# Kernel optimization log

Measured on AMD Instinct MI355X. Metric: run time of the kernel, lower is better.

The kernel has to match this reference:

```python
import jax, jax.numpy as jnp
import numpy as np

N = 50000      # nodes
E = 800000     # edges (avg degree 16)
F = 6          # input node features
C = 64         # conv_hidden_channels
M = 256        # mlp_hidden_channels
NCLS = 24      # num_classes
EPS = 1e-5     # BatchNorm eps


def _bn(h, g, b):
    # BatchNorm1d in training mode: biased batch stats over the batch axis
    mu = h.mean(axis=0)
    var = ((h - mu) ** 2).mean(axis=0)
    return g * (h - mu) * jax.lax.rsqrt(var + EPS) + b


def _block(x, W, b, g, beta):
    # Lin -> ReLU -> BN  (one MLP block)
    return _bn(jax.nn.relu(x @ W + b), g, beta)


def _edge_conv(x, src, dst, Wa, ba, ga, bea, Wb, bb, gb, beb):
    # EdgeConv: message = MLP([x_i, x_j - x_i]), max-aggregated onto target i
    xi = x[dst]                                   # [E, d]
    xj = x[src]                                   # [E, d]
    e = jnp.concatenate([xi, xj - xi], axis=-1)   # [E, 2d]
    h = _block(_block(e, Wa, ba, ga, bea), Wb, bb, gb, beb)  # [E, C]
    agg = jax.ops.segment_max(h, dst, num_segments=N)        # [N, C]
    return jnp.where(jnp.isfinite(agg), agg, 0.0)  # zero-fill isolated nodes


def setup_inputs() -> dict:
    key = jax.random.key(0)
    ks = jax.random.split(key, 12)

    def w(k, shape, fan_in):
        return jax.random.normal(k, shape, jnp.float32) * (1.0 / np.sqrt(fan_in))

    z = lambda *s: jnp.zeros(s, jnp.float32)
    o = lambda *s: jnp.ones(s, jnp.float32)

    x = jax.random.normal(ks[0], (N, F), jnp.float32)
    edge_index = jax.random.randint(ks[1], (2, E), 0, N, jnp.int32)

    return {
        "x": x,
        # conv1 MLP: Lin(2F,C)+BN, Lin(C,C)+BN
        "W1a": w(ks[2], (2 * F, C), 2 * F), "b1a": z(C), "g1a": o(C), "be1a": z(C),
        "W1b": w(ks[3], (C, C), C),         "b1b": z(C), "g1b": o(C), "be1b": z(C),
        # conv2/conv3 stacked: Lin(2C,C)+BN, Lin(C,C)+BN
        "Wa": w(ks[4], (2, 2 * C, C), 2 * C), "ba": z(2, C), "ga": o(2, C), "bea": z(2, C),
        "Wb": w(ks[5], (2, C, C), C),         "bb": z(2, C), "gb": o(2, C), "beb": z(2, C),
        # lin1: Lin(3C, M)+BN
        "Wl": w(ks[6], (3 * C, M), 3 * C), "bl": z(M), "gl": o(M), "bel": z(M),
        # head: Lin(M, M/4)+BN, Lin(M/4, M/8)+BN, Lin(M/8, NCLS)
        "Wm1": w(ks[7], (M, M // 4), M),      "bm1": z(M // 4), "gm1": o(M // 4), "bem1": z(M // 4),
        "Wm2": w(ks[8], (M // 4, M // 8), M // 4), "bm2": z(M // 8), "gm2": o(M // 8), "bem2": z(M // 8),
        "Wo": w(ks[9], (M // 8, NCLS), M // 8), "bo": z(NCLS),
        "edge_index": edge_index,
    }


def reference(x, W1a, b1a, g1a, be1a, W1b, b1b, g1b, be1b,
              Wa, ba, ga, bea, Wb, bb, gb, beb,
              Wl, bl, gl, bel,
              Wm1, bm1, gm1, bem1, Wm2, bm2, gm2, bem2,
              Wo, bo, edge_index):
    src, dst = edge_index[0], edge_index[1]
    x1 = _edge_conv(x,  src, dst, W1a, b1a, g1a, be1a, W1b, b1b, g1b, be1b)
    x2 = _edge_conv(x1, src, dst, Wa[0], ba[0], ga[0], bea[0], Wb[0], bb[0], gb[0], beb[0])
    x3 = _edge_conv(x2, src, dst, Wa[1], ba[1], ga[1], bea[1], Wb[1], bb[1], gb[1], beb[1])
    h = _block(jnp.concatenate([x1, x2, x3], axis=-1), Wl, bl, gl, bel)
    h = _block(h, Wm1, bm1, gm1, bem1)   # Dropout is identity (eval)
    h = _block(h, Wm2, bm2, gm2, bem2)   # Dropout is identity (eval)
    logits = h @ Wo + bo
    return jax.nn.log_softmax(logits, axis=1)
```

## Files before the change

### kernel.cpp

```cpp
#include <hip/hip_runtime.h>
#include <hip/hip_bf16.h>

#define EPS 1e-5f
typedef unsigned short bfr;
typedef unsigned short hfr;
typedef _Float16 h2v __attribute__((ext_vector_type(2)));
typedef _Float16 f16x8 __attribute__((ext_vector_type(8)));
typedef float f32x4 __attribute__((ext_vector_type(4)));

#if defined(__has_builtin)
#if __has_builtin(__builtin_amdgcn_fdot2)
#define HAS_FDOT2 1
#endif
#endif

static inline int cdiv(int a, int b){ return (a + b - 1) / b; }
static inline int imin(int a, int b){ return a < b ? a : b; }

__device__ __forceinline__ float bf2f(bfr u){ return __uint_as_float((unsigned)u << 16); }
__device__ __forceinline__ bfr f2bf(float f){
  unsigned u = __float_as_uint(f);
  u += 0x7fffu + ((u >> 16) & 1u);
  return (bfr)(u >> 16);
}
__device__ __forceinline__ unsigned pack2bf(float a, float b){
  return (unsigned)f2bf(a) | ((unsigned)f2bf(b) << 16);
}
__device__ __forceinline__ float h2f(hfr u){ _Float16 h; __builtin_memcpy(&h, &u, 2); return (float)h; }
__device__ __forceinline__ hfr f2h(float f){ _Float16 h = (_Float16)f; hfr u; __builtin_memcpy(&u, &h, 2); return u; }
__device__ __forceinline__ unsigned pack2h(float a, float b){
  return (unsigned)f2h(a) | ((unsigned)f2h(b) << 16);
}
__device__ __forceinline__ h2v u2h2(unsigned u){ h2v r; __builtin_memcpy(&r, &u, 4); return r; }
__device__ __forceinline__ unsigned h22u(h2v h){ unsigned u; __builtin_memcpy(&u, &h, 4); return u; }
__device__ __forceinline__ float dot2(h2v a, h2v b, float c){
#ifdef HAS_FDOT2
  return __builtin_amdgcn_fdot2(a, b, c, false);
#else
  return c + (float)a.x * (float)b.x + (float)a.y * (float)b.y;
#endif
}

__global__ __launch_bounds__(256) void detect_kernel(const bfr* __restrict__ xr, int nwords, int* __restrict__ flag){
  int i = threadIdx.x;
  int bad = 0;
  if (i < nwords){
    bfr lo = xr[2 * i];
    int e = (lo >> 7) & 0xFF;
    bool plausible = ((lo & 0x7FFF) == 0) || (e >= 97 && e <= 157);
    bad = plausible ? 0 : 1;
  }
  __shared__ int s[256];
  s[threadIdx.x] = bad; __syncthreads();
  for (int st = 128; st; st >>= 1){
    if (threadIdx.x < st) s[threadIdx.x] += s[threadIdx.x + st];
    __syncthreads();
  }
  if (threadIdx.x == 0) *flag = (s[0] > 32) ? 1 : 0;
}

#define NPAR 31
struct ParamPtrs { const void* p[NPAR]; };
struct ParamOfs  { int off[NPAR + 1]; };

__global__ __launch_bounds__(256) void acvt_batch_kernel(ParamPtrs pp, ParamOfs po,
                                                         float* __restrict__ out, int total,
                                                         const int* __restrict__ flag){
  int g = blockIdx.x * 256 + threadIdx.x;
  if (g >= total) return;
  int isf = *flag;
  int t = 0;
  while (po.off[t + 1] <= g) ++t;
  int i = g - po.off[t];
  out[g] = isf ? ((const float*)pp.p[t])[i] : bf2f(((const bfr*)pp.p[t])[i]);
}

__global__ __launch_bounds__(256) void deg_kernel(const int* __restrict__ dst, int* __restrict__ deg, int E){
  int e = blockIdx.x * 256 + threadIdx.x;
  if (e < E) atomicAdd(&deg[dst[e]], 1);
}

__global__ __launch_bounds__(256) void scan1_kernel(const int* __restrict__ deg, int* __restrict__ locoff,
                                                    int* __restrict__ bsum, int N){
  __shared__ int s[256];
  int i = blockIdx.x * 256 + threadIdx.x;
  int v = (i < N) ? deg[i] : 0;
  s[threadIdx.x] = v; __syncthreads();
  for (int st = 1; st < 256; st <<= 1){
    int u = (threadIdx.x >= st) ? s[threadIdx.x - st] : 0;
    __syncthreads();
    s[threadIdx.x] += u;
    __syncthreads();
  }
  if (i < N) locoff[i] = s[threadIdx.x] - v;
  if (threadIdx.x == 255) bsum[blockIdx.x] = s[255];
}

__global__ __launch_bounds__(256) void scan2_kernel(int* __restrict__ bsum, int nb){
  __shared__ int s[256];
  const int t = threadIdx.x;
  int carry = 0;
  for (int base = 0; base < nb; base += 256){
    int v = (base + t < nb) ? bsum[base + t] : 0;
    s[t] = v; __syncthreads();
    for (int st = 1; st < 256; st <<= 1){
      int u = (t >= st) ? s[t - st] : 0;
      __syncthreads();
      s[t] += u;
      __syncthreads();
    }
    if (base + t < nb) bsum[base + t] = carry + s[t] - v;
    carry += s[255];
    __syncthreads();
  }
}

__global__ __launch_bounds__(256) void scan3_kernel(const int* __restrict__ locoff, const int* __restrict__ bsum,
                                                    int* __restrict__ row_off, int* __restrict__ cur,
                                                    int N, int E){
  int i = blockIdx.x * 256 + threadIdx.x;
  if (i < N){
    int v = locoff[i] + bsum[blockIdx.x];
    row_off[i] = v; cur[i] = v;
  }
  if (i == 0) row_off[N] = E;
}

__global__ __launch_bounds__(256) void scatter_kernel(const int* __restrict__ src, const int* __restrict__ dst,
                                                      int* __restrict__ cur, int* __restrict__ ssrc, int E){
  int e = blockIdx.x * 256 + threadIdx.x;
  if (e < E){
    int d = dst[e];
    int p = atomicAdd(&cur[d], 1);
    ssrc[p] = src[e];
  }
}

template<bool FIRST>
__global__ __launch_bounds__(256) void gemmPQ_kernel(const void* __restrict__ Av, int lda,
                                                     const float* __restrict__ Wa, int d,
                                                     const float* __restrict__ ba,
                                                     hfr* __restrict__ P, hfr* __restrict__ Q, int N){
  __shared__ unsigned WsU[64 * 64];
  const int y = blockIdx.y;
  const int tot = d * 64;
  if (FIRST){
    float* Ws = (float*)WsU;
    for (int i = threadIdx.x; i < tot; i += 256)
      Ws[i] = y ? Wa[tot + i] : (Wa[i] - Wa[tot + i]);
  } else {
    for (int i = threadIdx.x; i < 32 * 64; i += 256){
      int p = i >> 6, c = i & 63;
      int i0 = (2 * p) * 64 + c, i1 = (2 * p + 1) * 64 + c;
      float w0 = y ? Wa[tot + i0] : (Wa[i0] - Wa[tot + i0]);
      float w1 = y ? Wa[tot + i1] : (Wa[i1] - Wa[tot + i1]);
      WsU[i] = pack2h(w0, w1);
    }
  }
  __syncthreads();
  const int row = blockIdx.x * 256 + threadIdx.x;
  if (row >= N) return;
  float acc[64];
#pragma unroll
  for (int c = 0; c < 64; ++c) acc[c] = 0.f;
  if (FIRST){
    const float* Ws = (const float*)WsU;
    const float* Af = (const float*)Av + (size_t)row * lda;
    for (int k = 0; k < d; ++k){
      float a = Af[k];
      const float* wr = Ws + k * 64;
#pragma unroll
      for (int c4 = 0; c4 < 16; ++c4){
        float4 w = *(const float4*)(wr + 4 * c4);
        acc[4*c4+0] += a * w.x; acc[4*c4+1] += a * w.y;
        acc[4*c4+2] += a * w.z; acc[4*c4+3] += a * w.w;
      }
    }
  } else {
    const hfr* Ah = (const hfr*)Av + (size_t)row * lda;
#pragma unroll
    for (int k8 = 0; k8 < 8; ++k8){
      uint4 av = *(const uint4*)(Ah + k8 * 8);
      unsigned pr[4] = {av.x, av.y, av.z, av.w};
#pragma unroll
      for (int pi = 0; pi < 4; ++pi){
        h2v ap = u2h2(pr[pi]);
        const unsigned* wr = WsU + (k8 * 4 + pi) * 64;
#pragma unroll
        for (int c = 0; c < 64; ++c) acc[c] = dot2(ap, u2h2(wr[c]), acc[c]);
      }
    }
  }
  if (!y){
#pragma unroll
    for (int c = 0; c < 64; ++c) acc[c] += ba[c];
  }
  unsigned p[32];
#pragma unroll
  for (int c = 0; c < 64; c += 2) p[c / 2] = pack2h(acc[c], acc[c + 1]);
  hfr* outp = (y ? Q : P) + (size_t)row * 64;
  uint4* op = (uint4*)outp;
#pragma unroll
  for (int i = 0; i < 8; ++i) op[i] = make_uint4(p[4*i], p[4*i+1], p[4*i+2], p[4*i+3]);
}

template<int NOUT, int KSTEPS, bool FOLD, bool PQ>
__global__ __launch_bounds__(256) void mgemm_kernel(const hfr* __restrict__ Ah, int lda,
                                                    const float* __restrict__ Wp0, const float* __restrict__ Wm0, int ldw,
                                                    const float* __restrict__ bias0,
                                                    const float* __restrict__ stats, float cntInv,
                                                    const float* __restrict__ g, const float* __restrict__ be,
                                                    hfr* __restrict__ Ov0, hfr* __restrict__ Ov1, int ldo,
                                                    int nrows, int relu){
  constexpr int K  = KSTEPS * 32;
  constexpr int KP = K + 8;
  constexpr int NT = NOUT / 16;
  __shared__ __align__(16) _Float16 W2T[NOUT * KP];
  __shared__ __align__(16) _Float16 etile[4][16][NOUT + 8];
  __shared__ float aS[FOLD ? K : 1], bbS[FOLD ? K : 1], bsum[FOLD ? 256 : 1];
  __shared__ float bfull[NOUT];
  const int tid = threadIdx.x;
  const int lane = tid & 63;
  const int wib = tid >> 6;
  const float* Wp = Wp0;
  const float* Wm = Wm0;
  const float* bias = bias0;
  hfr* Ov = Ov0;
  int colbase = blockIdx.y * NOUT;
  if (PQ){
    colbase = 0;
    if (blockIdx.y == 1){ Wp = Wp0 + (size_t)K * ldw; Wm = nullptr; bias = nullptr; Ov = Ov1; }
    else { Wm = Wp0 + (size_t)K * ldw; }
  }

  if (FOLD){
    for (int k = tid; k < K; k += 256){
      float mu = stats[k] * cntInv;
      float var = stats[K + k] * cntInv - mu * mu;
      float ai = g[k] * rsqrtf(var + EPS);
      aS[k] = ai; bbS[k] = be[k] - ai * mu;
    }
    __syncthreads();
  }
  for (int i = tid; i < K * NOUT; i += 256){
    int k = i / NOUT, c = i - k * NOUT;
    float w = Wp[(size_t)k * ldw + colbase + c];
    if (Wm) w -= Wm[(size_t)k * ldw + colbase + c];
    if (FOLD) w *= aS[k];
    W2T[c * KP + k] = (_Float16)w;
  }
  if (FOLD){
    constexpr int parts = 256 / NOUT;
    int c = tid % NOUT, p = tid / NOUT;
    float s = 0.f;
    for (int k = p; k < K; k += parts) s += bbS[k] * Wp[(size_t)k * ldw + colbase + c];
    bsum[p * NOUT + c] = s;
    __syncthreads();
    if (tid < NOUT){
      float t = bias[colbase + tid];
#pragma unroll
      for (int pp = 0; pp < parts; ++pp) t += bsum[pp * NOUT + tid];
      bfull[tid] = t;
    }
  } else {
    if (tid < NOUT) bfull[tid] = bias ? bias[colbase + tid] : 0.f;
  }
  __syncthreads();

  f16x8 Bf[KSTEPS][NT];
#pragma unroll
  for (int s = 0; s < KSTEPS; ++s)
#pragma unroll
    for (int t = 0; t < NT; ++t)
      Bf[s][t] = *(const f16x8*)&W2T[(t * 16 + (lane & 15)) * KP + s * 32 + (lane >> 4) * 8];
  float bc[NT];
#pragma unroll
  for (int t = 0; t < NT; ++t) bc[t] = bfull[t * 16 + (lane & 15)];

  const int ntiles = (nrows + 63) >> 6;
  for (int tile = blockIdx.x; tile < ntiles; tile += gridDim.x){
    const int r0 = tile * 64 + wib * 16;
    const int rowA = min(r0 + (lane & 15), nrows - 1);
    const hfr* Ap = Ah + (size_t)rowA * lda + (lane >> 4) * 8;
    f32x4 acc[NT];
#pragma unroll
    for (int t = 0; t < NT; ++t) acc[t] = (f32x4){bc[t], bc[t], bc[t], bc[t]};
#pragma unroll
    for (int s = 0; s < KSTEPS; ++s){
      f16x8 Af = *(const f16x8*)(Ap + s * 32);
#pragma unroll
      for (int t = 0; t < NT; ++t)
        acc[t] = __builtin_amdgcn_mfma_f32_16x16x32_f16(Af, Bf[s][t], acc[t], 0, 0, 0);
    }
#pragma unroll
    for (int t = 0; t < NT; ++t){
#pragma unroll
      for (int r = 0; r < 4; ++r){
        float v = acc[t][r];
        v = relu ? fmaxf(v, 0.f) : v;
        etile[wib][(lane >> 4) * 4 + r][t * 16 + (lane & 15)] = (_Float16)v;
      }
    }
    if (NOUT == 64){
#pragma unroll
      for (int h = 0; h < 2; ++h){
        int rl = h * 8 + (lane >> 3);
        int ch = lane & 7;
        uint4 vv = *(const uint4*)&etile[wib][rl][ch * 8];
        int rg = r0 + rl;
        if (rg < nrows) *(uint4*)(Ov + (size_t)rg * ldo + colbase + ch * 8) = vv;
      }
    } else {
      int rl = lane >> 2;
      int ch = lane & 3;
      uint4 vv = *(const uint4*)&etile[wib][rl][ch * 8];
      int rg = r0 + rl;
      if (rg < nrows) *(uint4*)(Ov + (size_t)rg * ldo + colbase + ch * 8) = vv;
    }
  }
}

__global__ __launch_bounds__(256) void passA_kernel(const hfr* __restrict__ P, const hfr* __restrict__ Q,
                                                    const int* __restrict__ ssrc, const int* __restrict__ row_off,
                                                    float* __restrict__ stats, hfr* __restrict__ h1, int N){
  const int tid = threadIdx.x;
  const int lane = tid & 63;
  const int wib = tid >> 6;
  const int er0 = lane >> 3;
  const int ck = lane & 7;
  const int wid = (blockIdx.x * 256 + tid) >> 6;
  const int nw = (gridDim.x * 256) >> 6;
  const _Float16 z16 = (_Float16)0;
  float s8[8], q8[8];
#pragma unroll
  for (int j = 0; j < 8; ++j){ s8[j] = 0.f; q8[j] = 0.f; }
  for (int n = wid; n < N; n += nw){
    const int e0 = row_off[n], e1 = row_off[n + 1];
    if (e0 >= e1) continue;
    uint4 pv4 = ((const uint4*)(P + (size_t)n * 64))[ck];
    h2v pp0 = u2h2(pv4.x), pp1 = u2h2(pv4.y), pp2 = u2h2(pv4.z), pp3 = u2h2(pv4.w);
    const int lim = e1 - 1;
    for (int eb = e0; eb < e1; eb += 16){
      int sv = ssrc[min(eb + (lane & 15), lim)];
#pragma unroll
      for (int h = 0; h < 2; ++h){
        int er = h * 8 + er0;
        int ge = eb + er;
        int sj = __shfl(sv, er, 64);
        uint4 qv = *((const uint4*)(Q + (size_t)sj * 64) + ck);
        h2v s0 = u2h2(qv.x) + pp0;
        h2v s1 = u2h2(qv.y) + pp1;
        h2v s2 = u2h2(qv.z) + pp2;
        h2v s3 = u2h2(qv.w) + pp3;
        s0.x = (s0.x < z16) ? z16 : s0.x; s0.y = (s0.y < z16) ? z16 : s0.y;
        s1.x = (s1.x < z16) ? z16 : s1.x; s1.y = (s1.y < z16) ? z16 : s1.y;
        s2.x = (s2.x < z16) ? z16 : s2.x; s2.y = (s2.y < z16) ? z16 : s2.y;
        s3.x = (s3.x < z16) ? z16 : s3.x; s3.y = (s3.y < z16) ? z16 : s3.y;
        if (ge < e1){
          *(uint4*)(h1 + (size_t)ge * 64 + ck * 8) = make_uint4(h22u(s0), h22u(s1), h22u(s2), h22u(s3));
          float v;
          v = (float)s0.x; s8[0] += v; q8[0] = fmaf(v, v, q8[0]);
          v = (float)s0.y; s8[1] += v; q8[1] = fmaf(v, v, q8[1]);
          v = (float)s1.x; s8[2] += v; q8[2] = fmaf(v, v, q8[2]);
          v = (float)s1.y; s8[3] += v; q8[3] = fmaf(v, v, q8[3]);
          v = (float)s2.x; s8[4] += v; q8[4] = fmaf(v, v, q8[4]);
          v = (float)s2.y; s8[5] += v; q8[5] = fmaf(v, v, q8[5]);
          v = (float)s3.x; s8[6] += v; q8[6] = fmaf(v, v, q8[6]);
          v = (float)s3.y; s8[7] += v; q8[7] = fmaf(v, v, q8[7]);
        }
      }
    }
  }
#pragma unroll
  for (int j = 0; j < 8; ++j){
    float s = s8[j], q = q8[j];
    s += __shfl_xor(s, 8, 64);  q += __shfl_xor(q, 8, 64);
    s += __shfl_xor(s, 16, 64); q += __shfl_xor(q, 16, 64);
    s += __shfl_xor(s, 32, 64); q += __shfl_xor(q, 32, 64);
    s8[j] = s; q8[j] = q;
  }
  __shared__ float ls[4][64], lq[4][64];
  if (lane < 8){
#pragma unroll
    for (int j = 0; j < 8; ++j){ ls[wib][lane * 8 + j] = s8[j]; lq[wib][lane * 8 + j] = q8[j]; }
  }
  __syncthreads();
  if (tid < 64){
    atomicAdd(&stats[tid], ls[0][tid] + ls[1][tid] + ls[2][tid] + ls[3][tid]);
  } else if (tid < 128){
    int c = tid - 64;
    atomicAdd(&stats[64 + c], lq[0][c] + lq[1][c] + lq[2][c] + lq[3][c]);
  }
}

__global__ __launch_bounds__(256) void passBC_kernel(const hfr* __restrict__ h1,
                                                     const int* __restrict__ row_off,
                                                     const float* __restrict__ statsIn, float Einv,
                                                     const float* __restrict__ g1, const float* __restrict__ be1,
                                                     const float* __restrict__ Wb, const float* __restrict__ bn,
                                                     float* __restrict__ agg, float* __restrict__ statsOut, int N){
  __shared__ __align__(16) _Float16 W2T[64 * 72];
  __shared__ float aS[64], bbS[64], b2S[64], bsum[256], qsum[256];
  const int tid = threadIdx.x;
  const int lane = tid & 63;
  if (tid < 64){
    float mu = statsIn[tid] * Einv;
    float var = statsIn[64 + tid] * Einv - mu * mu;
    float ai = g1[tid] * rsqrtf(var + EPS);
    aS[tid] = ai; bbS[tid] = be1[tid] - ai * mu;
  }
  __syncthreads();
  for (int i = tid; i < 4096; i += 256){
    int c = i >> 6, k = i & 63;
    W2T[c * 72 + k] = (_Float16)(aS[k] * Wb[(size_t)k * 64 + c]);
  }
  {
    int c = tid & 63, p = tid >> 6;
    float s = 0.f;
    for (int k = p; k < 64; k += 4) s += bbS[k] * Wb[(size_t)k * 64 + c];
    bsum[p * 64 + c] = s;
  }
  __syncthreads();
  if (tid < 64) b2S[tid] = bn[tid] + bsum[tid] + bsum[64 + tid] + bsum[128 + tid] + bsum[192 + tid];
  __syncthreads();
  f16x8 Bf[4][2];
#pragma unroll
  for (int t = 0; t < 4; ++t)
#pragma unroll
    for (int h = 0; h < 2; ++h){
      int c = t * 16 + (lane & 15);
      Bf[t][h] = *(const f16x8*)&W2T[c * 72 + h * 32 + (lane >> 4) * 8];
    }
  float bc[4];
#pragma unroll
  for (int t = 0; t < 4; ++t) bc[t] = b2S[t * 16 + (lane & 15)];
  const int wid = (blockIdx.x * 256 + tid) >> 6;
  const int nw = (gridDim.x * 256) >> 6;
  float sumT[4] = {0.f,0.f,0.f,0.f}, sqT[4] = {0.f,0.f,0.f,0.f};
  for (int n = wid; n < N; n += nw){
    const int e0 = row_off[n], e1 = row_off[n + 1];
    if (e0 >= e1) continue;
    float mxT[4] = {0.f,0.f,0.f,0.f};
    for (int eb = e0; eb < e1; eb += 16){
      const hfr* ap = h1 + (size_t)(eb + (lane & 15)) * 64 + (lane >> 4) * 8;
      f16x8 A0 = *(const f16x8*)ap;
      f16x8 A1 = *(const f16x8*)(ap + 32);
#pragma unroll
      for (int t = 0; t < 4; ++t){
        f32x4 Cv = {bc[t], bc[t], bc[t], bc[t]};
        Cv = __builtin_amdgcn_mfma_f32_16x16x32_f16(A0, Bf[t][0], Cv, 0, 0, 0);
        Cv = __builtin_amdgcn_mfma_f32_16x16x32_f16(A1, Bf[t][1], Cv, 0, 0, 0);
#pragma unroll
        for (int r = 0; r < 4; ++r){
          int rowi = (lane >> 4) * 4 + r;
          float v = fmaxf(Cv[r], 0.f);
          v = ((eb + rowi) < e1) ? v : 0.f;
          mxT[t] = fmaxf(mxT[t], v);
          sumT[t] += v;
          sqT[t]  = fmaf(v, v, sqT[t]);
        }
      }
    }
#pragma unroll
    for (int t = 0; t < 4; ++t){
      float m = mxT[t];
      m = fmaxf(m, __shfl_xor(m, 16, 64));
      m = fmaxf(m, __shfl_xor(m, 32, 64));
      mxT[t] = m;
    }
    float outv = (lane < 16) ? mxT[0] : (lane < 32) ? mxT[1] : (lane < 48) ? mxT[2] : mxT[3];
    agg[(size_t)n * 64 + lane] = outv;
  }
#pragma unroll
  for (int t = 0; t < 4; ++t){
    float s = sumT[t], q = sqT[t];
    s += __shfl_xor(s, 16, 64); s += __shfl_xor(s, 32, 64);
    q += __shfl_xor(q, 16, 64); q += __shfl_xor(q, 32, 64);
    sumT[t] = s; sqT[t] = q;
  }
  float ssel = (lane < 16) ? sumT[0] : (lane < 32) ? sumT[1] : (lane < 48) ? sumT[2] : sumT[3];
  float qsel = (lane < 16) ? sqT[0]  : (lane < 32) ? sqT[1]  : (lane < 48) ? sqT[2]  : sqT[3];
  bsum[tid] = ssel; qsum[tid] = qsel;
  __syncthreads();
  if (tid < 64){
    atomicAdd(&statsOut[tid], bsum[tid] + bsum[64 + tid] + bsum[128 + tid] + bsum[192 + tid]);
  } else if (tid < 128){
    int c = tid - 64;
    atomicAdd(&statsOut[64 + c], qsum[c] + qsum[64 + c] + qsum[128 + c] + qsum[192 + c]);
  }
}

__global__ __launch_bounds__(256) void fixup_kernel(const float* __restrict__ agg, const int* __restrict__ deg,
                                                    const float* __restrict__ stats, float cntInv,
                                                    const float* __restrict__ g, const float* __restrict__ be,
                                                    hfr* __restrict__ xout, int ldx, int N){
  int t = blockIdx.x * 256 + threadIdx.x;
  if (t >= N * 64) return;
  int n = t >> 6, c = t & 63;
  float mu = stats[c] * cntInv;
  float var = stats[64 + c] * cntInv - mu * mu;
  float a = g[c] * rsqrtf(var + EPS);
  float b = be[c] - a * mu;
  float v = 0.f;
  if (deg[n] > 0) v = a * agg[t] + b;
  xout[(size_t)n * ldx + c] = f2h(v);
}

template<int C>
__global__ __launch_bounds__(256) void statsN_kernel(const hfr* __restrict__ u, float* __restrict__ stats, int N){
  constexpr int CH = C / 8;
  constexpr int RP = 256 / CH;
  const int ch = threadIdx.x % CH;
  const int j0 = threadIdx.x / CH;
  float s[8], q[8];
#pragma unroll
  for (int j = 0; j < 8; ++j){ s[j] = 0.f; q[j] = 0.f; }
  for (int r = blockIdx.x * RP + j0; r < N; r += gridDim.x * RP){
    uint4 v = *(const uint4*)(u + (size_t)r * C + ch * 8);
    unsigned w[4] = {v.x, v.y, v.z, v.w};
#pragma unroll
    for (int t = 0; t < 4; ++t){
      h2v p = u2h2(w[t]);
      float a = (float)p.x, b = (float)p.y;
      s[2*t]   += a; q[2*t]   = fmaf(a, a, q[2*t]);
      s[2*t+1] += b; q[2*t+1] = fmaf(b, b, q[2*t+1]);
    }
  }
  __shared__ float ls[256][9], lq[256][9];
#pragma unroll
  for (int j = 0; j < 8; ++j){ ls[threadIdx.x][j] = s[j]; lq[threadIdx.x][j] = q[j]; }
  __syncthreads();
  if (threadIdx.x < C){
    int c = threadIdx.x, ch2 = c >> 3, jj = c & 7;
    float ss = 0.f, qq = 0.f;
    for (int p = 0; p < RP; ++p){ ss += ls[p * CH + ch2][jj]; qq += lq[p * CH + ch2][jj]; }
    atomicAdd(&stats[c], ss); atomicAdd(&stats[C + c], qq);
  }
}

__global__ __launch_bounds__(256) void head_kernel(const hfr* __restrict__ u2,
                                                   const float* __restrict__ stats, float cntInv,
                                                   const float* __restrict__ g, const float* __restrict__ be,
                                                   const float* __restrict__ Wo, const float* __restrict__ bo,
                                                   void* __restrict__ out, int N, const int* __restrict__ flag){
  __shared__ float Ws[32 * 24];
  __shared__ float bs[24];
  __shared__ float aS[32], bbS[32];
  const int tid = threadIdx.x;
  if (tid < 32){
    float mu = stats[tid] * cntInv;
    float var = stats[32 + tid] * cntInv - mu * mu;
    float ai = g[tid] * rsqrtf(var + EPS);
    aS[tid] = ai; bbS[tid] = be[tid] - ai * mu;
  }
  __syncthreads();
  for (int i = tid; i < 32 * 24; i += 256){
    int k = i / 24, c = i - 24 * k;
    Ws[i] = aS[k] * Wo[(size_t)k * 24 + c];
  }
  if (tid < 24){
    float t = bo[tid];
    for (int k = 0; k < 32; ++k) t += bbS[k] * Wo[(size_t)k * 24 + tid];
    bs[tid] = t;
  }
  __syncthreads();
  int r = blockIdx.x * 256 + tid;
  if (r >= N) return;
  int isf = *flag;
  float l[24];
#pragma unroll
  for (int c = 0; c < 24; ++c) l[c] = bs[c];
  const hfr* up = u2 + (size_t)r * 32;
#pragma unroll
  for (int k = 0; k < 32; ++k){
    float v = h2f(up[k]);
#pragma unroll
    for (int c = 0; c < 24; ++c) l[c] += v * Ws[k * 24 + c];
  }
  float m = l[0];
#pragma unroll
  for (int c = 1; c < 24; ++c) m = fmaxf(m, l[c]);
  float s = 0.f;
#pragma unroll
  for (int c = 0; c < 24; ++c) s += expf(l[c] - m);
  float lse = m + logf(s);
  if (isf){
    float4* op = (float4*)((float*)out + (size_t)r * 24);
#pragma unroll
    for (int i = 0; i < 6; ++i)
      op[i] = make_float4(l[4*i] - lse, l[4*i+1] - lse, l[4*i+2] - lse, l[4*i+3] - lse);
  } else {
    unsigned p[12];
#pragma unroll
    for (int c = 0; c < 24; c += 2) p[c / 2] = pack2bf(l[c] - lse, l[c + 1] - lse);
    uint4* op = (uint4*)((bfr*)out + (size_t)r * 24);
#pragma unroll
    for (int i = 0; i < 3; ++i) op[i] = make_uint4(p[4*i], p[4*i+1], p[4*i+2], p[4*i+3]);
  }
}

extern "C" void kernel_launch(void* const* d_in, const int* in_sizes, int n_in,
                              void* d_out, int out_size, void* d_ws, size_t ws_size,
                              hipStream_t stream){
  const int N = in_sizes[0] / 6;
  const int E = in_sizes[31] / 2;
  const int* edge = (const int*)d_in[31];
  const int* src = edge;
  const int* dst = edge + E;

  size_t off = 0; char* basep = (char*)d_ws;
  auto alloc = [&](size_t bytes) -> void* {
    void* p = basep + off;
    off = (off + bytes + 255) & ~(size_t)255;
    return p;
  };
  float* stA  = (float*)alloc(1472 * 4);
  float* stN1 = stA + 768;
  float* stN2 = stA + 1280;
  float* stN3 = stA + 1408;
  int*   flag = (int*)  alloc(4);
  int*   deg  = (int*)  alloc((size_t)N * 4);
  int*   rowo = (int*)  alloc((size_t)(N + 1) * 4);
  int*   cur  = (int*)  alloc((size_t)N * 4);
  int*   loco = (int*)  alloc((size_t)N * 4);
  int*   bsc  = (int*)  alloc(1024 * 4);
  int*   ssrc = (int*)  alloc((size_t)E * 4);

  ParamPtrs pp; ParamOfs po;
  int hoff[32]; int total = 0;
  for (int s = 0; s < NPAR; ++s){
    int idx = (s < 30) ? (s + 1) : 0;
    pp.p[s] = d_in[idx];
    po.off[s] = total;
    hoff[idx] = total;
    total += in_sizes[idx];
  }
  po.off[NPAR] = total;
  float* pf = (float*)alloc((size_t)total * 4);

  hfr*   P    = (hfr*)  alloc((size_t)N * 64 * 2);
  hfr*   Qb   = (hfr*)  alloc((size_t)N * 64 * 2);
  float* agg  = (float*)alloc((size_t)N * 64 * 4);
  hfr*   xcat = (hfr*)  alloc((size_t)N * 192 * 2);
  hfr*   h1   = (hfr*)  alloc((size_t)(E + 16) * 64 * 2);
  hfr* u_l = (hfr*)P;
  hfr* u1  = xcat;
  hfr* u2  = xcat + (size_t)N * 64;
  (void)ws_size; (void)n_in; (void)out_size;

  dim3 B(256);
  detect_kernel<<<1, B, 0, stream>>>((const bfr*)d_in[0], 256, flag);
  acvt_batch_kernel<<<cdiv(total, 256), B, 0, stream>>>(pp, po, pf, total, flag);

  hipMemsetAsync(stA, 0, 1472 * 4, stream);
  hipMemsetAsync(deg, 0, (size_t)N * 4, stream);
  hipMemsetAsync(h1 + (size_t)E * 64, 0, 16 * 64 * 2, stream);
  deg_kernel<<<cdiv(E, 256), B, 0, stream>>>(dst, deg, E);
  const int NBn = cdiv(N, 256);
  scan1_kernel<<<NBn, B, 0, stream>>>(deg, loco, bsc, N);
  scan2_kernel<<<1, B, 0, stream>>>(bsc, NBn);
  scan3_kernel<<<NBn, B, 0, stream>>>(loco, bsc, rowo, cur, N, E);
  scatter_kernel<<<cdiv(E, 256), B, 0, stream>>>(src, dst, cur, ssrc, E);

  const int NB = cdiv(N, 256);
  const int ntiles = cdiv(N, 64);
  const int GWA = 2048, GWB = 2048;
  const float Einv = 1.f / (float)E;
  for (int k = 0; k < 3; ++k){
    const float *Wa_k, *ba_k, *ga_k, *bea_k, *Wb_k, *bb_k, *gb_k, *beb_k;
    if (k == 0){
      Wa_k = pf + hoff[1]; ba_k = pf + hoff[2]; ga_k = pf + hoff[3]; bea_k = pf + hoff[4];
      Wb_k = pf + hoff[5]; bb_k = pf + hoff[6]; gb_k = pf + hoff[7]; beb_k = pf + hoff[8];
    } else {
      int kk = k - 1;
      Wa_k = pf + hoff[9]  + (size_t)kk * 128 * 64;
      ba_k = pf + hoff[10] + kk * 64;
      ga_k = pf + hoff[11] + kk * 64;
      bea_k= pf + hoff[12] + kk * 64;
      Wb_k = pf + hoff[13] + (size_t)kk * 64 * 64;
      bb_k = pf + hoff[14] + kk * 64;
      gb_k = pf + hoff[15] + kk * 64;
      beb_k= pf + hoff[16] + kk * 64;
    }
    float* st1 = stA + k * 256;
    float* st2 = st1 + 128;
    if (k == 0){
      gemmPQ_kernel<true><<<dim3(NB, 2), B, 0, stream>>>(pf + hoff[0], 6, Wa_k, 6, ba_k, P, Qb, N);
    } else {
      mgemm_kernel<64, 2, false, true><<<dim3(imin(ntiles, 1024), 2), B, 0, stream>>>(
          xcat + (size_t)(k - 1) * 64, 192, Wa_k, nullptr, 64, ba_k,
          nullptr, 0.f, nullptr, nullptr, P, Qb, 64, N, 0);
    }
    passA_kernel<<<GWA, B, 0, stream>>>(P, Qb, ssrc, rowo, st1, h1, N);
    passBC_kernel<<<GWB, B, 0, stream>>>(h1, rowo, st1, Einv, ga_k, bea_k, Wb_k, bb_k,
                                         agg, st2, N);
    fixup_kernel<<<cdiv(N * 64, 256), B, 0, stream>>>(agg, deg, st2, Einv, gb_k, beb_k,
                                                      xcat + (size_t)k * 64, 192, N);
  }

  mgemm_kernel<64, 6, false, false><<<dim3(imin(ntiles, 256), 4), B, 0, stream>>>(
      xcat, 192, pf + hoff[17], nullptr, 256, pf + hoff[18],
      nullptr, 0.f, nullptr, nullptr, u_l, nullptr, 256, N, 1);
  statsN_kernel<256><<<512, B, 0, stream>>>(u_l, stN1, N);
  mgemm_kernel<32, 8, true, false><<<dim3(imin(ntiles, 512), 2), B, 0, stream>>>(
      u_l, 256, pf + hoff[21], nullptr, 64, pf + hoff[22],
      stN1, 1.f / (float)N, pf + hoff[19], pf + hoff[20], u1, nullptr, 64, N, 1);
  statsN_kernel<64><<<512, B, 0, stream>>>(u1, stN2, N);
  mgemm_kernel<32, 2, true, false><<<dim3(imin(ntiles, 1024), 1), B, 0, stream>>>(
      u1, 64, pf + hoff[25], nullptr, 32, pf + hoff[26],
      stN2, 1.f / (float)N, pf + hoff[23], pf + hoff[24], u2, nullptr, 32, N, 1);
  statsN_kernel<32><<<512, B, 0, stream>>>(u2, stN3, N);
  head_kernel<<<cdiv(N, 256), B, 0, stream>>>(u2, stN3, 1.f / (float)N, pf + hoff[27], pf + hoff[28],
                                              pf + hoff[29], pf + hoff[30], d_out, N, flag);
  (void)NB;
}
```

Baseline: 852.7 us.

## Split edge MLP second layer into flat edge-tiled GEMM plus segmented max-fixup

The second Lin+ReLU of each EdgeConv now runs over flat 16-edge tiles across all edges instead of per-destination-node tiles. This removes the padded, partially masked MFMA tiles and the load imbalance that come from variable node degree. The activations are written back in fp16 in place over h1, and a new segfix kernel does the per-node max, the BatchNorm affine and the zero-fill for isolated nodes in one pass. This replaces the float agg buffer and the separate fixup kernel. The cost is one extra E×64 fp16 write and read per layer, the max now being taken on fp16 values, and smaller grid sizes.

```diff
diff --git a/kernel.cpp b/kernel.cpp
--- a/kernel.cpp
+++ b/kernel.cpp
@@ -393,16 +393,17 @@
   }
 }
 
-__global__ __launch_bounds__(256) void passBC_kernel(const hfr* __restrict__ h1,
-                                                     const int* __restrict__ row_off,
+__global__ __launch_bounds__(256) void flatBC_kernel(const hfr* __restrict__ h1, hfr* __restrict__ h2,
                                                      const float* __restrict__ statsIn, float Einv,
                                                      const float* __restrict__ g1, const float* __restrict__ be1,
                                                      const float* __restrict__ Wb, const float* __restrict__ bn,
-                                                     float* __restrict__ agg, float* __restrict__ statsOut, int N){
+                                                     float* __restrict__ statsOut, int E){
   __shared__ __align__(16) _Float16 W2T[64 * 72];
+  __shared__ __align__(16) _Float16 et[4][16][72];
   __shared__ float aS[64], bbS[64], b2S[64], bsum[256], qsum[256];
   const int tid = threadIdx.x;
   const int lane = tid & 63;
+  const int wib = tid >> 6;
   if (tid < 64){
     float mu = statsIn[tid] * Einv;
     float var = statsIn[64 + tid] * Einv - mu * mu;
@@ -436,40 +437,36 @@
   for (int t = 0; t < 4; ++t) bc[t] = b2S[t * 16 + (lane & 15)];
   const int wid = (blockIdx.x * 256 + tid) >> 6;
   const int nw = (gridDim.x * 256) >> 6;
+  const int lm = lane & 15, lq2 = lane >> 4;
+  const int ntiles = (E + 15) >> 4;
   float sumT[4] = {0.f,0.f,0.f,0.f}, sqT[4] = {0.f,0.f,0.f,0.f};
-  for (int n = wid; n < N; n += nw){
-    const int e0 = row_off[n], e1 = row_off[n + 1];
-    if (e0 >= e1) continue;
-    float mxT[4] = {0.f,0.f,0.f,0.f};
-    for (int eb = e0; eb < e1; eb += 16){
-      const hfr* ap = h1 + (size_t)(eb + (lane & 15)) * 64 + (lane >> 4) * 8;
-      f16x8 A0 = *(const f16x8*)ap;
-      f16x8 A1 = *(const f16x8*)(ap + 32);
-#pragma unroll
-      for (int t = 0; t < 4; ++t){
-        f32x4 Cv = {bc[t], bc[t], bc[t], bc[t]};
-        Cv = __builtin_amdgcn_mfma_f32_16x16x32_f16(A0, Bf[t][0], Cv, 0, 0, 0);
-        Cv = __builtin_amdgcn_mfma_f32_16x16x32_f16(A1, Bf[t][1], Cv, 0, 0, 0);
-#pragma unroll
-        for (int r = 0; r < 4; ++r){
-          int rowi = (lane >> 4) * 4 + r;
-          float v = fmaxf(Cv[r], 0.f);
-          v = ((eb + rowi) < e1) ? v : 0.f;
-          mxT[t] = fmaxf(mxT[t], v);
-          sumT[t] += v;
-          sqT[t]  = fmaf(v, v, sqT[t]);
-        }
+  for (int tile = wid; tile < ntiles; tile += nw){
+    const int r0 = tile << 4;
+    const hfr* ap = h1 + (size_t)(r0 + lm) * 64 + lq2 * 8;
+    f16x8 A0 = *(const f16x8*)ap;
+    f16x8 A1 = *(const f16x8*)(ap + 32);
+    const bool full = (r0 + 16 <= E);
+#pragma unroll
+    for (int t = 0; t < 4; ++t){
+      f32x4 Cv = {bc[t], bc[t], bc[t], bc[t]};
+      Cv = __builtin_amdgcn_mfma_f32_16x16x32_f16(A0, Bf[t][0], Cv, 0, 0, 0);
+      Cv = __builtin_amdgcn_mfma_f32_16x16x32_f16(A1, Bf[t][1], Cv, 0, 0, 0);
+#pragma unroll
+      for (int r = 0; r < 4; ++r){
+        float v = fmaxf(Cv[r], 0.f);
+        if (!full) v = ((r0 + lq2 * 4 + r) < E) ? v : 0.f;
+        sumT[t] += v;
+        sqT[t]  = fmaf(v, v, sqT[t]);
+        et[wib][lq2 * 4 + r][t * 16 + lm] = (_Float16)v;
       }
     }
 #pragma unroll
-    for (int t = 0; t < 4; ++t){
-      float m = mxT[t];
-      m = fmaxf(m, __shfl_xor(m, 16, 64));
-      m = fmaxf(m, __shfl_xor(m, 32, 64));
-      mxT[t] = m;
-    }
-    float outv = (lane < 16) ? mxT[0] : (lane < 32) ? mxT[1] : (lane < 48) ? mxT[2] : mxT[3];
-    agg[(size_t)n * 64 + lane] = outv;
+    for (int hh = 0; hh < 2; ++hh){
+      int rl = hh * 8 + (lane >> 3);
+      int ch = lane & 7;
+      uint4 vv = *(const uint4*)&et[wib][rl][ch * 8];
+      *(uint4*)(h2 + (size_t)(r0 + rl) * 64 + ch * 8) = vv;
+    }
   }
 #pragma unroll
   for (int t = 0; t < 4; ++t){
@@ -490,20 +487,45 @@
   }
 }
 
-__global__ __launch_bounds__(256) void fixup_kernel(const float* __restrict__ agg, const int* __restrict__ deg,
-                                                    const float* __restrict__ stats, float cntInv,
-                                                    const float* __restrict__ g, const float* __restrict__ be,
-                                                    hfr* __restrict__ xout, int ldx, int N){
-  int t = blockIdx.x * 256 + threadIdx.x;
-  if (t >= N * 64) return;
-  int n = t >> 6, c = t & 63;
-  float mu = stats[c] * cntInv;
-  float var = stats[64 + c] * cntInv - mu * mu;
-  float a = g[c] * rsqrtf(var + EPS);
-  float b = be[c] - a * mu;
-  float v = 0.f;
-  if (deg[n] > 0) v = a * agg[t] + b;
-  xout[(size_t)n * ldx + c] = f2h(v);
+__global__ __launch_bounds__(256) void segfix_kernel(const hfr* __restrict__ h2,
+                                                     const int* __restrict__ row_off,
+                                                     const float* __restrict__ stats, float cntInv,
+                                                     const float* __restrict__ g, const float* __restrict__ be,
+                                                     hfr* __restrict__ xout, int ldx, int N){
+  __shared__ float aC[64], bC[64];
+  const int tid = threadIdx.x;
+  if (tid < 64){
+    float mu = stats[tid] * cntInv;
+    float var = stats[64 + tid] * cntInv - mu * mu;
+    float a = g[tid] * rsqrtf(var + EPS);
+    aC[tid] = a; bC[tid] = be[tid] - a * mu;
+  }
+  __syncthreads();
+  const int lane = tid & 63;
+  const int c32 = lane & 31;
+  const int half = lane >> 5;
+  const int wid = (blockIdx.x * 256 + tid) >> 6;
+  const int nw = (gridDim.x * 256) >> 6;
+  const float a0 = aC[2 * c32],     b0 = bC[2 * c32];
+  const float a1 = aC[2 * c32 + 1], b1 = bC[2 * c32 + 1];
+  for (int n = wid; n < N; n += nw){
+    const int e0 = row_off[n], e1 = row_off[n + 1];
+    h2v mx; mx.x = (_Float16)0; mx.y = (_Float16)0;
+    for (int e = e0 + half; e < e1; e += 2){
+      h2v v = u2h2(*(const unsigned*)(h2 + (size_t)e * 64 + c32 * 2));
+      mx.x = (v.x > mx.x) ? v.x : mx.x;
+      mx.y = (v.y > mx.y) ? v.y : mx.y;
+    }
+    unsigned om = (unsigned)__shfl_xor((int)h22u(mx), 32, 64);
+    h2v ov = u2h2(om);
+    mx.x = (ov.x > mx.x) ? ov.x : mx.x;
+    mx.y = (ov.y > mx.y) ? ov.y : mx.y;
+    if (half == 0){
+      float v0 = (e0 < e1) ? fmaf((float)mx.x, a0, b0) : 0.f;
+      float v1 = (e0 < e1) ? fmaf((float)mx.y, a1, b1) : 0.f;
+      *(unsigned*)(xout + (size_t)n * ldx + c32 * 2) = pack2h(v0, v1);
+    }
+  }
 }
 
 template<int C>
@@ -646,7 +668,7 @@
   hfr* u_l = (hfr*)P;
   hfr* u1  = xcat;
   hfr* u2  = xcat + (size_t)N * 64;
-  (void)ws_size; (void)n_in; (void)out_size;
+  (void)ws_size; (void)n_in; (void)out_size; (void)agg;
 
   dim3 B(256);
   detect_kernel<<<1, B, 0, stream>>>((const bfr*)d_in[0], 256, flag);
@@ -664,7 +686,7 @@
 
   const int NB = cdiv(N, 256);
   const int ntiles = cdiv(N, 64);
-  const int GWA = 2048, GWB = 2048;
+  const int GWA = 1024, GWB = 1024, GWS = 1024;
   const float Einv = 1.f / (float)E;
   for (int k = 0; k < 3; ++k){
     const float *Wa_k, *ba_k, *ga_k, *bea_k, *Wb_k, *bb_k, *gb_k, *beb_k;
@@ -692,10 +714,9 @@
           nullptr, 0.f, nullptr, nullptr, P, Qb, 64, N, 0);
     }
     passA_kernel<<<GWA, B, 0, stream>>>(P, Qb, ssrc, rowo, st1, h1, N);
-    passBC_kernel<<<GWB, B, 0, stream>>>(h1, rowo, st1, Einv, ga_k, bea_k, Wb_k, bb_k,
-                                         agg, st2, N);
-    fixup_kernel<<<cdiv(N * 64, 256), B, 0, stream>>>(agg, deg, st2, Einv, gb_k, beb_k,
-                                                      xcat + (size_t)k * 64, 192, N);
+    flatBC_kernel<<<GWB, B, 0, stream>>>(h1, h1, st1, Einv, ga_k, bea_k, Wb_k, bb_k, st2, E);
+    segfix_kernel<<<GWS, B, 0, stream>>>(h1, rowo, st2, Einv, gb_k, beb_k,
+                                         xcat + (size_t)k * 64, 192, N);
   }
 
   mgemm_kernel<64, 6, false, false><<<dim3(imin(ntiles, 256), 4), B, 0, stream>>>(
```

Result: no change. 856.3 us (+0.4%).
